# Kernel tuning notes

Hardware: AMD Instinct MI355X
Metric: run time of the kernel (lower is better)

## Reference

```python
import jax, jax.numpy as jnp
import numpy as np

N = 50000        # nodes
E_RAND = 800000  # random edges (self-loops appended -> E = 850000)
H = 8            # num_heads
D = 32           # h_feat_dim
IN = 128         # in_feat_dim
SM = 256         # sm_dim
SP = 128         # sp_dim
NEG_SLOPE = 0.2  # DGL GATv2Conv default


def setup_inputs() -> dict:
    key = jax.random.key(0)
    ks = jax.random.split(key, 16)
    s = 0.05
    self_loops = jnp.arange(N, dtype=jnp.int32)
    return {
        "sm_feats": jax.random.normal(ks[0], (N, SM), jnp.float32),
        "sp_feats": jax.random.normal(ks[1], (N, SP), jnp.float32),
        "src": jnp.concatenate([jax.random.randint(ks[2], (E_RAND,), 0, N, jnp.int32), self_loops]),
        "dst": jnp.concatenate([jax.random.randint(ks[3], (E_RAND,), 0, N, jnp.int32), self_loops]),
        # T1 / T2 linears
        "T1_w": jax.random.normal(ks[4], (SM, IN), jnp.float32) * s,
        "T1_b": jnp.zeros((IN,), jnp.float32),
        "T2_w": jax.random.normal(ks[5], (SP, IN), jnp.float32) * s,
        "T2_b": jnp.zeros((IN,), jnp.float32),
        # GATv2 layer 1: in = 2*IN
        "g1_src_w": jax.random.normal(ks[6], (2 * IN, H * D), jnp.float32) * s,
        "g1_dst_w": jax.random.normal(ks[7], (2 * IN, H * D), jnp.float32) * s,
        "g1_attn": jax.random.normal(ks[8], (H, D), jnp.float32) * s,
        "g1_bias": jnp.zeros((H * D,), jnp.float32),
        # GATv2 layer 2: in = D (after head-mean)
        "g2_src_w": jax.random.normal(ks[9], (D, H * D), jnp.float32) * s,
        "g2_dst_w": jax.random.normal(ks[10], (D, H * D), jnp.float32) * s,
        "g2_attn": jax.random.normal(ks[11], (H, D), jnp.float32) * s,
        "g2_bias": jnp.zeros((H * D,), jnp.float32),
    }


def gatv2_conv(x, src, dst, w_src, w_dst, attn, bias):
    # DGL GATv2Conv (share_weights=False, bias=True, no residual/activation)
    feat_src = (x @ w_src).reshape(-1, H, D)   # [N,H,D]
    feat_dst = (x @ w_dst).reshape(-1, H, D)   # [N,H,D]
    e = jax.nn.leaky_relu(feat_src[src] + feat_dst[dst], NEG_SLOPE)  # [E,H,D]
    score = jnp.einsum('ehd,hd->eh', e, attn)  # [E,H]
    # edge softmax over incoming edges per destination (self-loops ensure non-empty)
    smax = jax.ops.segment_max(score, dst, num_segments=N)           # [N,H]
    ex = jnp.exp(score - smax[dst])
    denom = jax.ops.segment_sum(ex, dst, num_segments=N)             # [N,H]
    alpha = ex / denom[dst]                                          # [E,H]
    out = jax.ops.segment_sum(alpha[:, :, None] * feat_src[src], dst, num_segments=N)  # [N,H,D]
    return out + bias.reshape(1, H, D)


def reference(sm_feats, sp_feats, src, dst,
              T1_w, T1_b, T2_w, T2_b,
              g1_src_w, g1_dst_w, g1_attn, g1_bias,
              g2_src_w, g2_dst_w, g2_attn, g2_bias):
    in_feat = jnp.concatenate([sm_feats @ T1_w + T1_b,
                               sp_feats @ T2_w + T2_b], axis=1)      # [N, 2*IN]
    h = gatv2_conv(in_feat, src, dst, g1_src_w, g1_dst_w, g1_attn, g1_bias)
    h = jax.nn.elu(h).mean(axis=1)                                   # [N, D]
    h = gatv2_conv(h, src, dst, g2_src_w, g2_dst_w, g2_attn, g2_bias)
    return h.mean(axis=1)                                            # [N, D]
```

## Files before the change

### kernel.cpp

```cpp
#include <hip/hip_runtime.h>
#include <hip/hip_fp16.h>


typedef unsigned int uint32;
typedef unsigned short u16;
typedef short short8 __attribute__((ext_vector_type(8)));
typedef float f32x4 __attribute__((ext_vector_type(4)));
typedef _Float16 f16x2 __attribute__((ext_vector_type(2)));

union H2 { f16x2 v; uint32 u; };

__device__ __forceinline__ uint32 bf_rne(uint32 u) { return (u + 0x7fffu + ((u >> 16) & 1u)) >> 16; }

__device__ __forceinline__ void split_trunc(float a, float b, uint32& h, uint32& l) {
  uint32 ua = __float_as_uint(a), ub = __float_as_uint(b);
  h = __builtin_amdgcn_perm(ub, ua, 0x07060302u);
  float ra = a - __uint_as_float(ua & 0xffff0000u);
  float rb = b - __uint_as_float(ub & 0xffff0000u);
  l = __builtin_amdgcn_perm(__float_as_uint(rb), __float_as_uint(ra), 0x07060302u);
}

__device__ __forceinline__ int wave_incl_scan(int x) {
  int lane = threadIdx.x & 63;
#pragma unroll
  for (int off = 1; off < 64; off <<= 1) {
    int t = __shfl_up(x, off, 64);
    if (lane >= off) x += t;
  }
  return x;
}

__global__ __launch_bounds__(256) void k_deg(const int* __restrict__ dst, int* __restrict__ deg, int E) {
  int e = blockIdx.x * 256 + threadIdx.x;
  if (e < E) atomicAdd(&deg[dst[e]], 1);
}

__global__ __launch_bounds__(256) void k_blkscan(const int* __restrict__ in, int* __restrict__ out,
                                                 int* __restrict__ blksum, int n) {
  __shared__ int wsum[4];
  int tid = threadIdx.x;
  int i0 = blockIdx.x * 1024 + tid * 4;
  int v0 = 0, v1 = 0, v2 = 0, v3 = 0;
  if (i0 + 3 < n) {
    int4 t = *(const int4*)(in + i0);
    v0 = t.x; v1 = t.y; v2 = t.z; v3 = t.w;
  } else {
    if (i0 < n) v0 = in[i0];
    if (i0 + 1 < n) v1 = in[i0 + 1];
    if (i0 + 2 < n) v2 = in[i0 + 2];
    if (i0 + 3 < n) v3 = in[i0 + 3];
  }
  int ts = v0 + v1 + v2 + v3;
  int incl = wave_incl_scan(ts);
  int lane = tid & 63, wid = tid >> 6;
  if (lane == 63) wsum[wid] = incl;
  __syncthreads();
  if (tid == 0) {
    int a = wsum[0], b = wsum[1], c = wsum[2], d = wsum[3];
    wsum[0] = 0; wsum[1] = a; wsum[2] = a + b; wsum[3] = a + b + c;
    blksum[blockIdx.x] = a + b + c + d;
  }
  __syncthreads();
  int excl = wsum[wid] + incl - ts;
  if (i0 + 3 < n) {
    int4 o; o.x = excl; o.y = excl + v0; o.z = excl + v0 + v1; o.w = excl + v0 + v1 + v2;
    *(int4*)(out + i0) = o;
  } else {
    if (i0 < n) out[i0] = excl;
    if (i0 + 1 < n) out[i0 + 1] = excl + v0;
    if (i0 + 2 < n) out[i0 + 2] = excl + v0 + v1;
    if (i0 + 3 < n) out[i0 + 3] = excl + v0 + v1 + v2;
  }
}

__global__ void k_scan_top(int* __restrict__ bs, int G) {
  int lane = threadIdx.x;
  int base = 0;
  for (int s = 0; s < G; s += 64) {
    int i = s + lane;
    int v = (i < G) ? bs[i] : 0;
    int incl = wave_incl_scan(v);
    if (i < G) bs[i] = base + incl - v;
    base += __shfl(incl, 63, 64);
  }
}

__global__ __launch_bounds__(256) void k_addoff(int* __restrict__ rp, const int* __restrict__ bs, int n, int Etot) {
  int i = blockIdx.x * 256 + threadIdx.x;
  if (i < n) rp[i] += bs[i >> 10];
  if (i == 0) rp[n] = Etot;
}

__global__ __launch_bounds__(256) void k_fill(const int* __restrict__ src, const int* __restrict__ dst,
                                              const int* __restrict__ rp, int* __restrict__ cnt,
                                              int* __restrict__ csr_src, int E) {
  int e = blockIdx.x * 256 + threadIdx.x;
  if (e < E) {
    int d = dst[e];
    int p = rp[d] + atomicAdd(&cnt[d], 1);
    csr_src[p] = src[e];
  }
}

__global__ __launch_bounds__(256) void k_precomb(const float* __restrict__ T1w, const float* __restrict__ T1b,
                                                 const float* __restrict__ T2w, const float* __restrict__ T2b,
                                                 const float* __restrict__ G1, const float* __restrict__ G2,
                                                 u16* __restrict__ Bh, u16* __restrict__ Bl,
                                                 float* __restrict__ cvec) {
  int bb = blockIdx.x;
  const float* G = (bb < 385) ? G1 : G2;
  int off = (bb < 385) ? 0 : 256;
  int r = (bb < 385) ? bb : bb - 385;
  int j = threadIdx.x;
  float acc = 0.f;
  if (r < 256) {
    for (int m = 0; m < 128; m++) acc += T1w[r * 128 + m] * G[m * 256 + j];
  } else if (r < 384) {
    int rr = r - 256;
    for (int m = 0; m < 128; m++) acc += T2w[rr * 128 + m] * G[(128 + m) * 256 + j];
  } else {
    for (int m = 0; m < 128; m++) acc += T1b[m] * G[m * 256 + j] + T2b[m] * G[(128 + m) * 256 + j];
    cvec[off + j] = acc;
    return;
  }
  uint32 u = __float_as_uint(acc);
  uint32 hi = bf_rne(u);
  float rest = acc - __uint_as_float(hi << 16);
  uint32 lo = __float_as_uint(rest) >> 16;
  int k = r, colabs = off + j;
  int kt = k >> 5, lq = (k >> 3) & 3, j8 = k & 7;
  int cb = colabs >> 7, colr = colabs & 127, ni = colr >> 4, lr = colr & 15;
  size_t idx = ((size_t)(((cb * 12 + kt) * 8 + ni) * 4 + lq) * 16 + lr) * 8 + j8;
  Bh[idx] = (u16)hi;
  Bl[idx] = (u16)lo;
}

#define GLL(GP, LP)                                                     \
  __builtin_amdgcn_global_load_lds(                                     \
      (const __attribute__((address_space(1))) void*)(GP),              \
      (__attribute__((address_space(3))) void*)(LP), 16, 0, 0)

__global__ __launch_bounds__(256, 2) void k_gemm(const float* __restrict__ sm, const float* __restrict__ sp,
                                                 const u16* __restrict__ Bth, const u16* __restrict__ Btl,
                                                 const float* __restrict__ cvec, __half* __restrict__ fs,
                                                 __half* __restrict__ fd, int N) {
  __shared__ u16 BH[2][8192];
  __shared__ u16 BL[2][8192];
  int tid = threadIdx.x, w = tid >> 6, l = tid & 63;
  int lr = l & 15, lq = l >> 4;
  int L = blockIdx.x;
  int x = L & 7, m = L >> 3;
  int cb = m & 3;
  int rb = x + 8 * (m >> 2);
  int col0 = cb * 128, row0 = rb * 128;
  if (row0 >= N) return;
  int r0 = row0 + w * 32 + lr;
  int r1 = r0 + 16;
  int c0 = r0 < N ? r0 : N - 1;
  int c1 = r1 < N ? r1 : N - 1;
  const float* psm0 = sm + (size_t)c0 * 256 + lq * 8;
  const float* psm1 = sm + (size_t)c1 * 256 + lq * 8;
  const float* psp0 = sp + (size_t)c0 * 128 + lq * 8;
  const float* psp1 = sp + (size_t)c1 * 128 + lq * 8;

  f32x4 acc[2][8];
#pragma unroll
  for (int mt = 0; mt < 2; mt++)
#pragma unroll
    for (int ni = 0; ni < 8; ni++) acc[mt][ni] = (f32x4){0.f, 0.f, 0.f, 0.f};

#define STAGE_B(S, BUF)                                                 \
  {                                                                     \
    size_t g0 = (size_t)(cb * 12 + (S)*2) * 4096;                       \
    _Pragma("unroll") for (int i = 0; i < 4; i++) {                     \
      int c = i * 256 + tid;                                            \
      int lb = (i * 4 + w) * 512;                                       \
      GLL(Bth + g0 + (size_t)c * 8, &BH[BUF][lb]);                      \
      GLL(Btl + g0 + (size_t)c * 8, &BL[BUF][lb]);                      \
    }                                                                   \
  }

#define LOADA(P, D)                                                     \
  {                                                                     \
    const float* _g0 = ((P) < 8) ? (psm0 + (P)*32) : (psp0 + ((P)-8) * 32); \
    const float* _g1 = ((P) < 8) ? (psm1 + (P)*32) : (psp1 + ((P)-8) * 32); \
    D[0] = *(const float4*)_g0;                                         \
    D[1] = *(const float4*)(_g0 + 4);                                   \
    D[2] = *(const float4*)_g1;                                         \
    D[3] = *(const float4*)(_g1 + 4);                                   \
  }

#define COMP(T, BUF, D)                                                 \
  {                                                                     \
    uint4 H0, L0, H1, L1;                                               \
    split_trunc(D[0].x, D[0].y, H0.x, L0.x);                            \
    split_trunc(D[0].z, D[0].w, H0.y, L0.y);                            \
    split_trunc(D[1].x, D[1].y, H0.z, L0.z);                            \
    split_trunc(D[1].z, D[1].w, H0.w, L0.w);                            \
    split_trunc(D[2].x, D[2].y, H1.x, L1.x);                            \
    split_trunc(D[2].z, D[2].w, H1.y, L1.y);                            \
    split_trunc(D[3].x, D[3].y, H1.z, L1.z);                            \
    split_trunc(D[3].z, D[3].w, H1.w, L1.w);                            \
    short8 a0h = *(short8*)&H0, a0l = *(short8*)&L0;                    \
    short8 a1h = *(short8*)&H1, a1l = *(short8*)&L1;                    \
    _Pragma("unroll") for (int ni = 0; ni < 8; ni++) {                  \
      int lo = (((T)*8 + ni) * 64 + l) * 8;                             \
      short8 bh = *(const short8*)&BH[BUF][lo];                         \
      short8 bl = *(const short8*)&BL[BUF][lo];                         \
      acc[0][ni] = __builtin_amdgcn_mfma_f32_16x16x32_bf16(a0h, bh, acc[0][ni], 0, 0, 0); \
      acc[0][ni] = __builtin_amdgcn_mfma_f32_16x16x32_bf16(a0l, bh, acc[0][ni], 0, 0, 0); \
      acc[0][ni] = __builtin_amdgcn_mfma_f32_16x16x32_bf16(a0h, bl, acc[0][ni], 0, 0, 0); \
      acc[1][ni] = __builtin_amdgcn_mfma_f32_16x16x32_bf16(a1h, bh, acc[1][ni], 0, 0, 0); \
      acc[1][ni] = __builtin_amdgcn_mfma_f32_16x16x32_bf16(a1l, bh, acc[1][ni], 0, 0, 0); \
      acc[1][ni] = __builtin_amdgcn_mfma_f32_16x16x32_bf16(a1h, bl, acc[1][ni], 0, 0, 0); \
    }                                                                   \
  }

  float4 A[2][8];
  STAGE_B(0, 0);
  LOADA(0, A[0]);
  LOADA(1, (A[0] + 4));

#pragma unroll
  for (int st = 0; st < 6; st++) {
    const int cu = st & 1, nx = cu ^ 1;
    __syncthreads();
    if (st < 5) {
      STAGE_B(st + 1, nx);
      LOADA(2 * st + 2, A[nx]);
      LOADA(2 * st + 3, (A[nx] + 4));
    }
    COMP(0, cu, A[cu]);
    COMP(1, cu, (A[cu] + 4));
  }

#pragma unroll
  for (int mt = 0; mt < 2; mt++) {
    int rbr = row0 + w * 32 + mt * 16 + lq * 4;
#pragma unroll
    for (int ni = 0; ni < 8; ni++) {
      int c = col0 + ni * 16 + lr;
      float cv = cvec[c];
      __half* op = fs; int cc = c;
      if (c >= 256) { op = fd; cc = c - 256; }
#pragma unroll
      for (int r = 0; r < 4; r++) {
        int rr = rbr + r;
        if (rr < N) op[(size_t)rr * 256 + cc] = __float2half(acc[mt][ni][r] + cv);
      }
    }
  }
#undef STAGE_B
#undef LOADA
#undef COMP
}

__global__ __launch_bounds__(256) void k_feat2(const float* __restrict__ h, const float* __restrict__ Ws,
                                               const float* __restrict__ Wd, __half* __restrict__ fs,
                                               __half* __restrict__ fd, int N) {
  int j = threadIdx.x;
  int n0 = blockIdx.x * 32;
  float ws[32], wd[32];
#pragma unroll
  for (int k = 0; k < 32; k++) {
    ws[k] = Ws[k * 256 + j];
    wd[k] = Wd[k * 256 + j];
  }
  int nend = n0 + 32; if (nend > N) nend = N;
#pragma unroll 2
  for (int n = n0; n < nend; n++) {
    const float* hr = h + (size_t)n * 32;
    float as = 0.f, ad = 0.f;
#pragma unroll
    for (int k = 0; k < 32; k++) {
      float hv = hr[k];
      as += hv * ws[k];
      ad += hv * wd[k];
    }
    fs[(size_t)n * 256 + j] = __float2half(as);
    fd[(size_t)n * 256 + j] = __float2half(ad);
  }
}

template <int FINAL>
__global__ __launch_bounds__(256) void k_edge(const uint2* __restrict__ fs, const uint2* __restrict__ fd,
                                              const int* __restrict__ csr_src, const int* __restrict__ rp,
                                              const float* __restrict__ attn, const float* __restrict__ bias,
                                              float* __restrict__ out, int N) {
  int n = blockIdx.x * 4 + (threadIdx.x >> 6);
  if (n >= N) return;
  int lane = threadIdx.x & 63;
  float4 av = ((const float4*)attn)[lane];
  H2 AV01, AV23, Y01, Y23;
  AV01.v = (f16x2){(_Float16)av.x, (_Float16)av.y};
  AV23.v = (f16x2){(_Float16)av.z, (_Float16)av.w};
  const f16x2 c02 = {(_Float16)0.2f, (_Float16)0.2f};
  uint2 yu = fd[(size_t)n * 64 + lane];
  Y01.u = yu.x; Y23.u = yu.y;
  int beg = rp[n], end = rp[n + 1];
  float den0 = 0.f, den1 = 0.f;
  float4 acc0 = {0.f, 0.f, 0.f, 0.f}, acc1 = {0.f, 0.f, 0.f, 0.f};

  auto edge1 = [&](uint2 xu, float& den, float4& acc) {
    H2 Xa, Xb; Xa.u = xu.x; Xb.u = xu.y;
    f16x2 ea = Xa.v + Y01.v, eb = Xb.v + Y23.v;
    f16x2 ta = __builtin_elementwise_max(ea, ea * c02);
    f16x2 tb = __builtin_elementwise_max(eb, eb * c02);
    float p = __builtin_amdgcn_fdot2(ta, AV01.v, 0.f, false);
    p = __builtin_amdgcn_fdot2(tb, AV23.v, p, false);
    p += __shfl_xor(p, 1, 64);
    p += __shfl_xor(p, 2, 64);
    p += __shfl_xor(p, 4, 64);
    float wgt = __expf(p);
    den += wgt;
    acc.x += wgt * (float)Xa.v.x; acc.y += wgt * (float)Xa.v.y;
    acc.z += wgt * (float)Xb.v.x; acc.w += wgt * (float)Xb.v.y;
  };

  int e = beg;
  int nq = (end - beg) >> 2;
  if (nq > 0) {
    int s0 = csr_src[e], s1 = csr_src[e + 1], s2 = csr_src[e + 2], s3 = csr_src[e + 3];
    uint2 x0 = fs[(size_t)s0 * 64 + lane];
    uint2 x1 = fs[(size_t)s1 * 64 + lane];
    uint2 x2 = fs[(size_t)s2 * 64 + lane];
    uint2 x3 = fs[(size_t)s3 * 64 + lane];
    for (int q = 1; q < nq; q++) {
      int b2 = e + 4 * q;
      int t0 = csr_src[b2], t1 = csr_src[b2 + 1], t2 = csr_src[b2 + 2], t3 = csr_src[b2 + 3];
      uint2 y0 = fs[(size_t)t0 * 64 + lane];
      uint2 y1 = fs[(size_t)t1 * 64 + lane];
      uint2 y2 = fs[(size_t)t2 * 64 + lane];
      uint2 y3 = fs[(size_t)t3 * 64 + lane];
      edge1(x0, den0, acc0); edge1(x1, den1, acc1);
      edge1(x2, den0, acc0); edge1(x3, den1, acc1);
      x0 = y0; x1 = y1; x2 = y2; x3 = y3;
    }
    edge1(x0, den0, acc0); edge1(x1, den1, acc1);
    edge1(x2, den0, acc0); edge1(x3, den1, acc1);
    e += 4 * nq;
  }
  for (; e < end; e++) {
    int s0 = csr_src[e];
    uint2 xu = fs[(size_t)s0 * 64 + lane];
    edge1(xu, den0, acc0);
  }

  float4 acc = {acc0.x + acc1.x, acc0.y + acc1.y, acc0.z + acc1.z, acc0.w + acc1.w};
  float invd = 1.f / (den0 + den1);
  float4 b = ((const float4*)bias)[lane];
  acc.x = acc.x * invd + b.x;
  acc.y = acc.y * invd + b.y;
  acc.z = acc.z * invd + b.z;
  acc.w = acc.w * invd + b.w;
  if (!FINAL) {
    acc.x = acc.x > 0.f ? acc.x : expm1f(acc.x);
    acc.y = acc.y > 0.f ? acc.y : expm1f(acc.y);
    acc.z = acc.z > 0.f ? acc.z : expm1f(acc.z);
    acc.w = acc.w > 0.f ? acc.w : expm1f(acc.w);
  }
#pragma unroll
  for (int mask = 8; mask <= 32; mask <<= 1) {
    acc.x += __shfl_xor(acc.x, mask, 64);
    acc.y += __shfl_xor(acc.y, mask, 64);
    acc.z += __shfl_xor(acc.z, mask, 64);
    acc.w += __shfl_xor(acc.w, mask, 64);
  }
  if (lane < 8) {
    float4 o = {acc.x * 0.125f, acc.y * 0.125f, acc.z * 0.125f, acc.w * 0.125f};
    ((float4*)out)[(size_t)n * 8 + lane] = o;
  }
}

extern "C" void kernel_launch(void* const* d_in, const int* in_sizes, int n_in,
                              void* d_out, int out_size, void* d_ws, size_t ws_size,
                              hipStream_t stream) {
  const float* sm  = (const float*)d_in[0];
  const float* sp  = (const float*)d_in[1];
  const int*   src = (const int*)d_in[2];
  const int*   dst = (const int*)d_in[3];
  const float* T1w = (const float*)d_in[4];
  const float* T1b = (const float*)d_in[5];
  const float* T2w = (const float*)d_in[6];
  const float* T2b = (const float*)d_in[7];
  const float* g1sw = (const float*)d_in[8];
  const float* g1dw = (const float*)d_in[9];
  const float* g1a  = (const float*)d_in[10];
  const float* g1b  = (const float*)d_in[11];
  const float* g2sw = (const float*)d_in[12];
  const float* g2dw = (const float*)d_in[13];
  const float* g2a  = (const float*)d_in[14];
  const float* g2b  = (const float*)d_in[15];
  const int N = in_sizes[1] / 128;
  const int E = in_sizes[2];
  float* out = (float*)d_out;

  size_t off = 0;
  char* wsb = (char*)d_ws;
  auto alloc = [&](size_t bytes) -> void* {
    void* p = wsb + off;
    off += (bytes + 255) & ~(size_t)255;
    return p;
  };
  u16* Bth = (u16*)alloc((size_t)512 * 384 * 2);
  u16* Btl = (u16*)alloc((size_t)512 * 384 * 2);
  float* cvec  = (float*)alloc(512 * 4);
  int* deg     = (int*)alloc((size_t)N * 4);
  int* cnt     = (int*)alloc((size_t)N * 4);
  int* row_ptr = (int*)alloc((size_t)(N + 1) * 4);
  int* blksum  = (int*)alloc(4096 * 4);
  int* csr_src = (int*)alloc((size_t)E * 4);
  __half* fs   = (__half*)alloc((size_t)N * 256 * 2);
  __half* fd   = (__half*)alloc((size_t)N * 256 * 2);
  float* hmid  = (float*)alloc((size_t)N * 32 * 4);
  (void)ws_size; (void)n_in; (void)out_size;

  (void)hipMemsetAsync(deg, 0, (size_t)N * 4, stream);
  (void)hipMemsetAsync(cnt, 0, (size_t)N * 4, stream);

  k_deg<<<(E + 255) / 256, 256, 0, stream>>>(dst, deg, E);
  int nblk = (N + 1023) / 1024;
  k_blkscan<<<nblk, 256, 0, stream>>>(deg, row_ptr, blksum, N);
  k_scan_top<<<1, 64, 0, stream>>>(blksum, nblk);
  k_addoff<<<(N + 255) / 256, 256, 0, stream>>>(row_ptr, blksum, N, E);
  k_fill<<<(E + 255) / 256, 256, 0, stream>>>(src, dst, row_ptr, cnt, csr_src, E);

  k_precomb<<<770, 256, 0, stream>>>(T1w, T1b, T2w, T2b, g1sw, g1dw, Bth, Btl, cvec);

  int rbs = (N + 127) / 128;
  int rbp = (rbs + 7) & ~7;
  k_gemm<<<dim3(rbp * 4), 256, 0, stream>>>(sm, sp, Bth, Btl, cvec, fs, fd, N);
  k_edge<0><<<(N + 3) / 4, 256, 0, stream>>>((const uint2*)fs, (const uint2*)fd, csr_src, row_ptr, g1a, g1b, hmid, N);

  k_feat2<<<(N + 31) / 32, 256, 0, stream>>>(hmid, g2sw, g2dw, fs, fd, N);
  k_edge<1><<<(N + 3) / 4, 256, 0, stream>>>((const uint2*)fs, (const uint2*)fd, csr_src, row_ptr, g2a, g2b, out, N);
}
```

Before: 498.5 us.

## Retile fused input GEMM to 256x64 blocks with per-half A prefetch

Changes the GEMM block tile from 128 rows x 128 cols to 256 rows x 64 cols. Each wave now covers 64 rows and 4 column tiles, and the pre-combined weight layout is rearranged to 64-column blocks to match. The fp32 A operand loads are split into two register halves, so the next K-slice is prefetched while the current one is computed. The goal is to cut the number of times the large fp32 activation matrix is reread across column blocks and to shrink LDS per block. The cost is more blocks each loading B, higher A register pressure, and less prefetch distance for A.

New measurement: 517.4 us. +3.8%, slower.

```diff
diff --git a/kernel.cpp b/kernel.cpp
--- a/kernel.cpp
+++ b/kernel.cpp
@@ -129,8 +129,8 @@
   uint32 lo = __float_as_uint(rest) >> 16;
   int k = r, colabs = off + j;
   int kt = k >> 5, lq = (k >> 3) & 3, j8 = k & 7;
-  int cb = colabs >> 7, colr = colabs & 127, ni = colr >> 4, lr = colr & 15;
-  size_t idx = ((size_t)(((cb * 12 + kt) * 8 + ni) * 4 + lq) * 16 + lr) * 8 + j8;
+  int cb = colabs >> 6, colr = colabs & 63, ni = colr >> 4, lr = colr & 15;
+  size_t idx = ((size_t)(((cb * 12 + kt) * 4 + ni) * 4 + lq) * 16 + lr) * 8 + j8;
   Bh[idx] = (u16)hi;
   Bl[idx] = (u16)lo;
 }
@@ -144,35 +144,37 @@
                                                  const u16* __restrict__ Bth, const u16* __restrict__ Btl,
                                                  const float* __restrict__ cvec, __half* __restrict__ fs,
                                                  __half* __restrict__ fd, int N) {
-  __shared__ u16 BH[2][8192];
-  __shared__ u16 BL[2][8192];
+  __shared__ u16 BH[2][4096];
+  __shared__ u16 BL[2][4096];
   int tid = threadIdx.x, w = tid >> 6, l = tid & 63;
   int lr = l & 15, lq = l >> 4;
   int L = blockIdx.x;
-  int x = L & 7, m = L >> 3;
-  int cb = m & 3;
-  int rb = x + 8 * (m >> 2);
-  int col0 = cb * 128, row0 = rb * 128;
+  int x = L & 7, m5 = L >> 3;
+  int cb = m5 & 7;
+  int rb = x + 8 * (m5 >> 3);
+  int col0 = cb * 64, row0 = rb * 256;
   if (row0 >= N) return;
-  int r0 = row0 + w * 32 + lr;
-  int r1 = r0 + 16;
-  int c0 = r0 < N ? r0 : N - 1;
-  int c1 = r1 < N ? r1 : N - 1;
-  const float* psm0 = sm + (size_t)c0 * 256 + lq * 8;
-  const float* psm1 = sm + (size_t)c1 * 256 + lq * 8;
-  const float* psp0 = sp + (size_t)c0 * 128 + lq * 8;
-  const float* psp1 = sp + (size_t)c1 * 128 + lq * 8;
-
-  f32x4 acc[2][8];
-#pragma unroll
-  for (int mt = 0; mt < 2; mt++)
-#pragma unroll
-    for (int ni = 0; ni < 8; ni++) acc[mt][ni] = (f32x4){0.f, 0.f, 0.f, 0.f};
+  int rbase = row0 + w * 64 + lr;
+  const float* psm[4];
+  const float* psp[4];
+#pragma unroll
+  for (int m = 0; m < 4; m++) {
+    int r = rbase + m * 16;
+    int cix = r < N ? r : N - 1;
+    psm[m] = sm + (size_t)cix * 256 + lq * 8;
+    psp[m] = sp + (size_t)cix * 128 + lq * 8;
+  }
+
+  f32x4 acc[4][4];
+#pragma unroll
+  for (int mt = 0; mt < 4; mt++)
+#pragma unroll
+    for (int ni = 0; ni < 4; ni++) acc[mt][ni] = (f32x4){0.f, 0.f, 0.f, 0.f};
 
 #define STAGE_B(S, BUF)                                                 \
   {                                                                     \
-    size_t g0 = (size_t)(cb * 12 + (S)*2) * 4096;                       \
-    _Pragma("unroll") for (int i = 0; i < 4; i++) {                     \
+    size_t g0 = (size_t)(cb * 12 + (S)*2) * 2048;                       \
+    _Pragma("unroll") for (int i = 0; i < 2; i++) {                     \
       int c = i * 256 + tid;                                            \
       int lb = (i * 4 + w) * 512;                                       \
       GLL(Bth + g0 + (size_t)c * 8, &BH[BUF][lb]);                      \
@@ -182,63 +184,55 @@
 
 #define LOADA(P, D)                                                     \
   {                                                                     \
-    const float* _g0 = ((P) < 8) ? (psm0 + (P)*32) : (psp0 + ((P)-8) * 32); \
-    const float* _g1 = ((P) < 8) ? (psm1 + (P)*32) : (psp1 + ((P)-8) * 32); \
-    D[0] = *(const float4*)_g0;                                         \
-    D[1] = *(const float4*)(_g0 + 4);                                   \
-    D[2] = *(const float4*)_g1;                                         \
-    D[3] = *(const float4*)(_g1 + 4);                                   \
+    _Pragma("unroll") for (int m = 0; m < 4; m++) {                     \
+      const float* _g = ((P) < 8) ? (psm[m] + (P)*32) : (psp[m] + ((P)-8) * 32); \
+      D[2 * m] = *(const float4*)_g;                                    \
+      D[2 * m + 1] = *(const float4*)(_g + 4);                          \
+    }                                                                   \
   }
 
 #define COMP(T, BUF, D)                                                 \
   {                                                                     \
-    uint4 H0, L0, H1, L1;                                               \
-    split_trunc(D[0].x, D[0].y, H0.x, L0.x);                            \
-    split_trunc(D[0].z, D[0].w, H0.y, L0.y);                            \
-    split_trunc(D[1].x, D[1].y, H0.z, L0.z);                            \
-    split_trunc(D[1].z, D[1].w, H0.w, L0.w);                            \
-    split_trunc(D[2].x, D[2].y, H1.x, L1.x);                            \
-    split_trunc(D[2].z, D[2].w, H1.y, L1.y);                            \
-    split_trunc(D[3].x, D[3].y, H1.z, L1.z);                            \
-    split_trunc(D[3].z, D[3].w, H1.w, L1.w);                            \
-    short8 a0h = *(short8*)&H0, a0l = *(short8*)&L0;                    \
-    short8 a1h = *(short8*)&H1, a1l = *(short8*)&L1;                    \
-    _Pragma("unroll") for (int ni = 0; ni < 8; ni++) {                  \
-      int lo = (((T)*8 + ni) * 64 + l) * 8;                             \
+    uint4 AH[4], AL[4];                                                 \
+    _Pragma("unroll") for (int m = 0; m < 4; m++) {                     \
+      split_trunc(D[2 * m].x, D[2 * m].y, AH[m].x, AL[m].x);            \
+      split_trunc(D[2 * m].z, D[2 * m].w, AH[m].y, AL[m].y);            \
+      split_trunc(D[2 * m + 1].x, D[2 * m + 1].y, AH[m].z, AL[m].z);    \
+      split_trunc(D[2 * m + 1].z, D[2 * m + 1].w, AH[m].w, AL[m].w);    \
+    }                                                                   \
+    _Pragma("unroll") for (int ni = 0; ni < 4; ni++) {                  \
+      int lo = (((T)*4 + ni) * 64 + l) * 8;                             \
       short8 bh = *(const short8*)&BH[BUF][lo];                         \
       short8 bl = *(const short8*)&BL[BUF][lo];                         \
-      acc[0][ni] = __builtin_amdgcn_mfma_f32_16x16x32_bf16(a0h, bh, acc[0][ni], 0, 0, 0); \
-      acc[0][ni] = __builtin_amdgcn_mfma_f32_16x16x32_bf16(a0l, bh, acc[0][ni], 0, 0, 0); \
-      acc[0][ni] = __builtin_amdgcn_mfma_f32_16x16x32_bf16(a0h, bl, acc[0][ni], 0, 0, 0); \
-      acc[1][ni] = __builtin_amdgcn_mfma_f32_16x16x32_bf16(a1h, bh, acc[1][ni], 0, 0, 0); \
-      acc[1][ni] = __builtin_amdgcn_mfma_f32_16x16x32_bf16(a1l, bh, acc[1][ni], 0, 0, 0); \
-      acc[1][ni] = __builtin_amdgcn_mfma_f32_16x16x32_bf16(a1h, bl, acc[1][ni], 0, 0, 0); \
+      _Pragma("unroll") for (int m = 0; m < 4; m++) {                   \
+        short8 ah = *(short8*)&AH[m], al = *(short8*)&AL[m];            \
+        acc[m][ni] = __builtin_amdgcn_mfma_f32_16x16x32_bf16(ah, bh, acc[m][ni], 0, 0, 0); \
+        acc[m][ni] = __builtin_amdgcn_mfma_f32_16x16x32_bf16(al, bh, acc[m][ni], 0, 0, 0); \
+        acc[m][ni] = __builtin_amdgcn_mfma_f32_16x16x32_bf16(ah, bl, acc[m][ni], 0, 0, 0); \
+      }                                                                 \
     }                                                                   \
   }
 
-  float4 A[2][8];
+  float4 Ra[8], Rb[8];
   STAGE_B(0, 0);
-  LOADA(0, A[0]);
-  LOADA(1, (A[0] + 4));
+  LOADA(0, Ra);
 
 #pragma unroll
   for (int st = 0; st < 6; st++) {
     const int cu = st & 1, nx = cu ^ 1;
     __syncthreads();
-    if (st < 5) {
-      STAGE_B(st + 1, nx);
-      LOADA(2 * st + 2, A[nx]);
-      LOADA(2 * st + 3, (A[nx] + 4));
-    }
-    COMP(0, cu, A[cu]);
-    COMP(1, cu, (A[cu] + 4));
-  }
-
-#pragma unroll
-  for (int mt = 0; mt < 2; mt++) {
-    int rbr = row0 + w * 32 + mt * 16 + lq * 4;
-#pragma unroll
-    for (int ni = 0; ni < 8; ni++) {
+    if (st < 5) STAGE_B(st + 1, nx);
+    LOADA(2 * st + 1, Rb);
+    COMP(0, cu, Ra);
+    if (st < 5) LOADA(2 * st + 2, Ra);
+    COMP(1, cu, Rb);
+  }
+
+#pragma unroll
+  for (int mt = 0; mt < 4; mt++) {
+    int rbr = row0 + w * 64 + mt * 16 + lq * 4;
+#pragma unroll
+    for (int ni = 0; ni < 4; ni++) {
       int c = col0 + ni * 16 + lr;
       float cv = cvec[c];
       __half* op = fs; int cc = c;
@@ -427,9 +421,9 @@
 
   k_precomb<<<770, 256, 0, stream>>>(T1w, T1b, T2w, T2b, g1sw, g1dw, Bth, Btl, cvec);
 
-  int rbs = (N + 127) / 128;
+  int rbs = (N + 255) / 256;
   int rbp = (rbs + 7) & ~7;
-  k_gemm<<<dim3(rbp * 4), 256, 0, stream>>>(sm, sp, Bth, Btl, cvec, fs, fd, N);
+  k_gemm<<<dim3(rbp * 8), 256, 0, stream>>>(sm, sp, Bth, Btl, cvec, fs, fd, N);
   k_edge<0><<<(N + 3) / 4, 256, 0, stream>>>((const uint2*)fs, (const uint2*)fd, csr_src, row_ptr, g1a, g1b, hmid, N);
 
   k_feat2<<<(N + 31) / 32, 256, 0, stream>>>(hmid, g2sw, g2dw, fs, fd, N);
```

## Halve GEMM K-stage size and drop A register prefetch to raise occupancy

Applied to the files above, without the earlier changes.

The projection GEMM now stages B in 32-wide K slices (half the LDS per buffer) across 12 stages instead of 64-wide slices across 6. The register double-buffer for A is removed: A is loaded at the top of each stage and consumed immediately. Launch bounds go from 2 to 4 blocks per CU. The goal is lower LDS and register use so more waves can hide latency, at the cost of twice as many barriers and A-load latency exposed inside each stage.

Measured after the change: 476.6 us. -4.4%, faster.

```diff
diff --git a/kernel.cpp b/kernel.cpp
--- a/kernel.cpp
+++ b/kernel.cpp
@@ -140,12 +140,12 @@
       (const __attribute__((address_space(1))) void*)(GP),              \
       (__attribute__((address_space(3))) void*)(LP), 16, 0, 0)
 
-__global__ __launch_bounds__(256, 2) void k_gemm(const float* __restrict__ sm, const float* __restrict__ sp,
+__global__ __launch_bounds__(256, 4) void k_gemm(const float* __restrict__ sm, const float* __restrict__ sp,
                                                  const u16* __restrict__ Bth, const u16* __restrict__ Btl,
                                                  const float* __restrict__ cvec, __half* __restrict__ fs,
                                                  __half* __restrict__ fd, int N) {
-  __shared__ u16 BH[2][8192];
-  __shared__ u16 BL[2][8192];
+  __shared__ u16 BH[2][4096];
+  __shared__ u16 BL[2][4096];
   int tid = threadIdx.x, w = tid >> 6, l = tid & 63;
   int lr = l & 15, lq = l >> 4;
   int L = blockIdx.x;
@@ -171,8 +171,8 @@
 
 #define STAGE_B(S, BUF)                                                 \
   {                                                                     \
-    size_t g0 = (size_t)(cb * 12 + (S)*2) * 4096;                       \
-    _Pragma("unroll") for (int i = 0; i < 4; i++) {                     \
+    size_t g0 = (size_t)(cb * 12 + (S)) * 4096;                         \
+    _Pragma("unroll") for (int i = 0; i < 2; i++) {                     \
       int c = i * 256 + tid;                                            \
       int lb = (i * 4 + w) * 512;                                       \
       GLL(Bth + g0 + (size_t)c * 8, &BH[BUF][lb]);                      \
@@ -180,58 +180,42 @@
     }                                                                   \
   }
 
-#define LOADA(P, D)                                                     \
-  {                                                                     \
-    const float* _g0 = ((P) < 8) ? (psm0 + (P)*32) : (psp0 + ((P)-8) * 32); \
-    const float* _g1 = ((P) < 8) ? (psm1 + (P)*32) : (psp1 + ((P)-8) * 32); \
-    D[0] = *(const float4*)_g0;                                         \
-    D[1] = *(const float4*)(_g0 + 4);                                   \
-    D[2] = *(const float4*)_g1;                                         \
-    D[3] = *(const float4*)(_g1 + 4);                                   \
-  }
-
-#define COMP(T, BUF, D)                                                 \
-  {                                                                     \
-    uint4 H0, L0, H1, L1;                                               \
-    split_trunc(D[0].x, D[0].y, H0.x, L0.x);                            \
-    split_trunc(D[0].z, D[0].w, H0.y, L0.y);                            \
-    split_trunc(D[1].x, D[1].y, H0.z, L0.z);                            \
-    split_trunc(D[1].z, D[1].w, H0.w, L0.w);                            \
-    split_trunc(D[2].x, D[2].y, H1.x, L1.x);                            \
-    split_trunc(D[2].z, D[2].w, H1.y, L1.y);                            \
-    split_trunc(D[3].x, D[3].y, H1.z, L1.z);                            \
-    split_trunc(D[3].z, D[3].w, H1.w, L1.w);                            \
-    short8 a0h = *(short8*)&H0, a0l = *(short8*)&L0;                    \
-    short8 a1h = *(short8*)&H1, a1l = *(short8*)&L1;                    \
-    _Pragma("unroll") for (int ni = 0; ni < 8; ni++) {                  \
-      int lo = (((T)*8 + ni) * 64 + l) * 8;                             \
-      short8 bh = *(const short8*)&BH[BUF][lo];                         \
-      short8 bl = *(const short8*)&BL[BUF][lo];                         \
-      acc[0][ni] = __builtin_amdgcn_mfma_f32_16x16x32_bf16(a0h, bh, acc[0][ni], 0, 0, 0); \
-      acc[0][ni] = __builtin_amdgcn_mfma_f32_16x16x32_bf16(a0l, bh, acc[0][ni], 0, 0, 0); \
-      acc[0][ni] = __builtin_amdgcn_mfma_f32_16x16x32_bf16(a0h, bl, acc[0][ni], 0, 0, 0); \
-      acc[1][ni] = __builtin_amdgcn_mfma_f32_16x16x32_bf16(a1h, bh, acc[1][ni], 0, 0, 0); \
-      acc[1][ni] = __builtin_amdgcn_mfma_f32_16x16x32_bf16(a1l, bh, acc[1][ni], 0, 0, 0); \
-      acc[1][ni] = __builtin_amdgcn_mfma_f32_16x16x32_bf16(a1h, bl, acc[1][ni], 0, 0, 0); \
-    }                                                                   \
-  }
-
-  float4 A[2][8];
   STAGE_B(0, 0);
-  LOADA(0, A[0]);
-  LOADA(1, (A[0] + 4));
-
-#pragma unroll
-  for (int st = 0; st < 6; st++) {
+
+#pragma unroll
+  for (int st = 0; st < 12; st++) {
     const int cu = st & 1, nx = cu ^ 1;
     __syncthreads();
-    if (st < 5) {
-      STAGE_B(st + 1, nx);
-      LOADA(2 * st + 2, A[nx]);
-      LOADA(2 * st + 3, (A[nx] + 4));
+    const float* ga0 = (st < 8) ? (psm0 + st * 32) : (psp0 + (st - 8) * 32);
+    const float* ga1 = (st < 8) ? (psm1 + st * 32) : (psp1 + (st - 8) * 32);
+    float4 v00 = *(const float4*)(ga0);
+    float4 v01 = *(const float4*)(ga0 + 4);
+    float4 v10 = *(const float4*)(ga1);
+    float4 v11 = *(const float4*)(ga1 + 4);
+    if (st < 11) STAGE_B(st + 1, nx);
+    uint4 H0, L0, H1, L1;
+    split_trunc(v00.x, v00.y, H0.x, L0.x);
+    split_trunc(v00.z, v00.w, H0.y, L0.y);
+    split_trunc(v01.x, v01.y, H0.z, L0.z);
+    split_trunc(v01.z, v01.w, H0.w, L0.w);
+    split_trunc(v10.x, v10.y, H1.x, L1.x);
+    split_trunc(v10.z, v10.w, H1.y, L1.y);
+    split_trunc(v11.x, v11.y, H1.z, L1.z);
+    split_trunc(v11.z, v11.w, H1.w, L1.w);
+    short8 a0h = *(short8*)&H0, a0l = *(short8*)&L0;
+    short8 a1h = *(short8*)&H1, a1l = *(short8*)&L1;
+#pragma unroll
+    for (int ni = 0; ni < 8; ni++) {
+      int lo = (ni * 64 + l) * 8;
+      short8 bh = *(const short8*)&BH[cu][lo];
+      short8 bl = *(const short8*)&BL[cu][lo];
+      acc[0][ni] = __builtin_amdgcn_mfma_f32_16x16x32_bf16(a0h, bh, acc[0][ni], 0, 0, 0);
+      acc[0][ni] = __builtin_amdgcn_mfma_f32_16x16x32_bf16(a0l, bh, acc[0][ni], 0, 0, 0);
+      acc[0][ni] = __builtin_amdgcn_mfma_f32_16x16x32_bf16(a0h, bl, acc[0][ni], 0, 0, 0);
+      acc[1][ni] = __builtin_amdgcn_mfma_f32_16x16x32_bf16(a1h, bh, acc[1][ni], 0, 0, 0);
+      acc[1][ni] = __builtin_amdgcn_mfma_f32_16x16x32_bf16(a1l, bh, acc[1][ni], 0, 0, 0);
+      acc[1][ni] = __builtin_amdgcn_mfma_f32_16x16x32_bf16(a1h, bl, acc[1][ni], 0, 0, 0);
     }
-    COMP(0, cu, A[cu]);
-    COMP(1, cu, (A[cu] + 4));
   }
 
 #pragma unroll
@@ -251,8 +235,6 @@
     }
   }
 #undef STAGE_B
-#undef LOADA
-#undef COMP
 }
 
 __global__ __launch_bounds__(256) void k_feat2(const float* __restrict__ h, const float* __restrict__ Ws,
```
